# Kernel tuning notes

Measured on AMD Instinct MI355X. Metric: run time of the kernel, lower is better.

The kernel has to match this reference:

```python
import jax, jax.numpy as jnp
import numpy as np

B, E = 256, 512
C, K = 8192, 10          # n_class, n_center
LMD = 10.0
INV_GAMMA = 10.0         # 1 / gamma, gamma = 0.1
TAU = 0.2
MARGIN = 0.01


def setup_inputs() -> dict:
    key = jax.random.key(0)
    k1, k2, k3 = jax.random.split(key, 3)
    embeddings = jax.random.normal(k1, (B, E), dtype=jnp.float32)
    labels = jax.random.randint(k2, (B,), 0, C, dtype=jnp.int64)
    fc = jax.random.normal(k3, (C * K, E), dtype=jnp.float32)
    return {"embeddings": embeddings, "labels": labels, "fc": fc}


def reference(embeddings, labels, fc):
    # L2-normalize centers (rows of fc), like F.normalize(fc, p=2, dim=1)
    norm = jnp.sqrt(jnp.sum(fc * fc, axis=1, keepdims=True))
    w = fc / jnp.maximum(norm, 1e-12)

    # similarity to every center: [B, C, K]
    x = (embeddings @ w.T).reshape(B, C, K)
    prob = jax.nn.softmax(INV_GAMMA * x, axis=2)
    h = jnp.sum(prob * x, axis=2)  # [B, C] soft-pooled class similarity

    # subtract margin on ground-truth class, then cross-entropy
    rows = jnp.arange(B)
    margin_m = jnp.zeros_like(h).at[rows, labels].set(MARGIN)
    logits = LMD * (h - margin_m)
    logp = jax.nn.log_softmax(logits, axis=1)
    loss_cls = -jnp.mean(logp[rows, labels])

    # regularizer: batched per-class center gram, replaces python loop over C
    wc = w.reshape(C, K, E)
    sub = 1.0 - jnp.einsum('cke,cje->ckj', wc, wc)   # [C, K, K]
    sub = jnp.where(sub <= 0.0, 1e-10, sub)
    mask = jnp.triu(jnp.ones((K, K), dtype=bool), k=1)  # strict upper triangle
    safe = jnp.where(mask, 2.0 * sub, 1.0)
    reg = jnp.sum(jnp.where(mask, jnp.sqrt(safe), 0.0))
    reg = reg / (C * K * (K - 1.0))
    return loss_cls + TAU * reg
```

## Files before the change

kernel.cpp:

```cpp
#include <hip/hip_runtime.h>


typedef __bf16 bf16;
typedef bf16 bf16x8 __attribute__((ext_vector_type(8)));
typedef float f32x4 __attribute__((ext_vector_type(4)));

#define NCLASS 8192
#define KC 10
#define EDIM 512
#define BATCH 256

__device__ inline void load_lds16(const void* g, void* l) {
    __builtin_amdgcn_global_load_lds(
        (const __attribute__((address_space(1))) void*)g,
        (__attribute__((address_space(3))) void*)l, 16, 0, 0);
}

__global__ __launch_bounds__(256) void prep_kernel(
    const float* __restrict__ fc, bf16* __restrict__ w,
    float* __restrict__ gram_part)
{
    __shared__ float rows[KC * EDIM];
    __shared__ float s_invn[KC];
    __shared__ float s_wsum[4];
    const int c = blockIdx.x;
    const int t = threadIdx.x;
    const int wave = t >> 6, lane = t & 63;

    const float4* src = (const float4*)(fc + (size_t)c * (KC * EDIM));
    float4* rows4 = (float4*)rows;
    #pragma unroll
    for (int i = 0; i < 5; ++i) rows4[t + i * 256] = src[t + i * 256];
    __syncthreads();

    for (int r = wave; r < KC; r += 4) {
        float s = 0.f;
        #pragma unroll
        for (int j = 0; j < 8; ++j) {
            float v = rows[r * EDIM + lane + j * 64];
            s += v * v;
        }
        #pragma unroll
        for (int off = 32; off; off >>= 1) s += __shfl_xor(s, off);
        if (lane == 0) s_invn[r] = 1.0f / fmaxf(sqrtf(s), 1e-12f);
    }
    __syncthreads();

    bf16x8* dst = (bf16x8*)(w + (size_t)c * (KC * EDIM));
    #pragma unroll
    for (int p = 0; p < 3; ++p) {
        int j = t + p * 256;
        if (j < 640) {
            int r = j >> 6;
            float inv = s_invn[r];
            float4 a = *(const float4*)(rows + j * 8);
            float4 b = *(const float4*)(rows + j * 8 + 4);
            bf16x8 v;
            v[0] = (bf16)(a.x * inv); v[1] = (bf16)(a.y * inv);
            v[2] = (bf16)(a.z * inv); v[3] = (bf16)(a.w * inv);
            v[4] = (bf16)(b.x * inv); v[5] = (bf16)(b.y * inv);
            v[6] = (bf16)(b.z * inv); v[7] = (bf16)(b.w * inv);
            dst[j] = v;
        }
    }

    float part = 0.f;
    for (int p = wave; p < 45; p += 4) {
        int i = 0, pp = p;
        while (pp >= 9 - i) { pp -= 9 - i; ++i; }
        int j = i + 1 + pp;
        float s = 0.f;
        #pragma unroll
        for (int u = 0; u < 8; ++u)
            s += rows[i * EDIM + lane + u * 64] * rows[j * EDIM + lane + u * 64];
        #pragma unroll
        for (int off = 32; off; off >>= 1) s += __shfl_xor(s, off);
        if (lane == 0) {
            float sub = 1.0f - s * s_invn[i] * s_invn[j];
            if (sub <= 0.0f) sub = 1e-10f;
            part += sqrtf(2.0f * sub);
        }
    }
    if (lane == 0) s_wsum[wave] = part;
    __syncthreads();
    if (t == 0) gram_part[c] = s_wsum[0] + s_wsum[1] + s_wsum[2] + s_wsum[3];
}

__global__ __launch_bounds__(256) void conv_kernel(
    const float* __restrict__ e, bf16* __restrict__ At)
{
    int i = blockIdx.x * 256 + threadIdx.x;
    int row = i >> 6, chunk = i & 63;
    int k = chunk * 8;
    float4 a = ((const float4*)e)[i * 2];
    float4 b = ((const float4*)e)[i * 2 + 1];
    bf16x8 v;
    v[0] = (bf16)a.x; v[1] = (bf16)a.y; v[2] = (bf16)a.z; v[3] = (bf16)a.w;
    v[4] = (bf16)b.x; v[5] = (bf16)b.y; v[6] = (bf16)b.z; v[7] = (bf16)b.w;
    *(bf16x8*)&At[((k >> 5) << 13) + (row << 5) + (k & 31)] = v;
}

__global__ __launch_bounds__(512, 2) void gemm_h_kernel(
    const bf16* __restrict__ W,
    const bf16* __restrict__ At,
    float* __restrict__ h)
{
    __shared__ bf16 Ws[80 * 32];
    const int tid = threadIdx.x;
    const int wave = tid >> 6, lane = tid & 63;

    f32x4 acc[5][2];
    #pragma unroll
    for (int mt = 0; mt < 5; ++mt)
        #pragma unroll
        for (int nt = 0; nt < 2; ++nt)
            acc[mt][nt] = (f32x4){0.f, 0.f, 0.f, 0.f};

    const size_t g0 = (size_t)blockIdx.x * 80;

    const int srow = tid >> 2;
    const int gc = (tid & 3) ^ ((srow >> 1) & 3);
    const bf16* wsrc = W + (g0 + srow) * EDIM + gc * 8;

    const int q = lane >> 4;
    const int q8 = q * 8;
    const int fr = lane & 15;

    for (int kb = 0; kb < EDIM; kb += 32) {
        if (tid < 320)
            load_lds16(wsrc + kb, Ws + wave * 64 * 8);
        __syncthreads();

        bf16x8 wf[5], ef[2];
        #pragma unroll
        for (int nt = 0; nt < 2; ++nt) {
            int row = wave * 32 + nt * 16 + fr;
            ef[nt] = *(const bf16x8*)
                &At[((kb >> 5) << 13) + (row << 5) + q8];
        }
        #pragma unroll
        for (int mt = 0; mt < 5; ++mt) {
            int row = mt * 16 + fr;
            int slot = q ^ ((row >> 1) & 3);
            wf[mt] = *(const bf16x8*)&Ws[row * 32 + slot * 8];
        }
        #pragma unroll
        for (int mt = 0; mt < 5; ++mt)
            #pragma unroll
            for (int nt = 0; nt < 2; ++nt)
                acc[mt][nt] = __builtin_amdgcn_mfma_f32_16x16x32_bf16(
                    wf[mt], ef[nt], acc[mt][nt], 0, 0, 0);
        __syncthreads();
    }

    const int col = lane & 15;
    const int quad = lane >> 4;
    const int cb = blockIdx.x * 8;
    #pragma unroll
    for (int nt = 0; nt < 2; ++nt) {
        int b = wave * 32 + nt * 16 + col;
        float hval[8];
        #pragma unroll
        for (int cc = 0; cc < 8; ++cc) {
            float xm = -1e30f;
            #pragma unroll
            for (int mt = 0; mt < 5; ++mt) {
                if (10 * cc + 10 > 16 * mt && 10 * cc < 16 * mt + 16) {
                    #pragma unroll
                    for (int rg = 0; rg < 4; ++rg) {
                        int r = 16 * mt + 4 * quad + rg;
                        if (r >= 10 * cc && r < 10 * cc + 10)
                            xm = fmaxf(xm, acc[mt][nt][rg]);
                    }
                }
            }
            xm = fmaxf(xm, __shfl_xor(xm, 16));
            xm = fmaxf(xm, __shfl_xor(xm, 32));
            float s1 = 0.f, s2 = 0.f;
            #pragma unroll
            for (int mt = 0; mt < 5; ++mt) {
                if (10 * cc + 10 > 16 * mt && 10 * cc < 16 * mt + 16) {
                    #pragma unroll
                    for (int rg = 0; rg < 4; ++rg) {
                        int r = 16 * mt + 4 * quad + rg;
                        if (r >= 10 * cc && r < 10 * cc + 10) {
                            float x = acc[mt][nt][rg];
                            float e = __expf(10.0f * (x - xm));
                            s1 += e; s2 += e * x;
                        }
                    }
                }
            }
            s1 += __shfl_xor(s1, 16); s1 += __shfl_xor(s1, 32);
            s2 += __shfl_xor(s2, 16); s2 += __shfl_xor(s2, 32);
            hval[cc] = s2 / s1;
        }
        if (quad == 0) {
            float4 v0 = {hval[0], hval[1], hval[2], hval[3]};
            float4 v1 = {hval[4], hval[5], hval[6], hval[7]};
            float4* dst = (float4*)&h[(size_t)b * NCLASS + cb];
            dst[0] = v0;
            dst[1] = v1;
        }
    }
}

__global__ __launch_bounds__(256) void ce_kernel(
    const float* __restrict__ h, const int* __restrict__ labels,
    float* __restrict__ ce_part)
{
    __shared__ float redm[4];
    __shared__ float reds[4];
    const int b = blockIdx.x, t = threadIdx.x;
    const int wave = t >> 6, lane = t & 63;
    const int lbl = labels[b];
    const float* hb = h + (size_t)b * NCLASS;

    float lg_cache[32];
    float mx = -1e30f;
    #pragma unroll
    for (int k = 0; k < 32; ++k) {
        int c = t + k * 256;
        float lg = 10.0f * hb[c];
        if (c == lbl) lg -= 0.1f;
        lg_cache[k] = lg;
        mx = fmaxf(mx, lg);
    }
    #pragma unroll
    for (int off = 32; off; off >>= 1) mx = fmaxf(mx, __shfl_xor(mx, off));
    if (lane == 0) redm[wave] = mx;
    __syncthreads();
    mx = fmaxf(fmaxf(redm[0], redm[1]), fmaxf(redm[2], redm[3]));

    float s = 0.f;
    #pragma unroll
    for (int k = 0; k < 32; ++k) s += __expf(lg_cache[k] - mx);
    #pragma unroll
    for (int off = 32; off; off >>= 1) s += __shfl_xor(s, off);
    if (lane == 0) reds[wave] = s;
    __syncthreads();
    if (t == 0) {
        s = reds[0] + reds[1] + reds[2] + reds[3];
        float logit_l = 10.0f * (hb[lbl] - 0.01f);
        ce_part[b] = mx + logf(s) - logit_l;
    }
}

__global__ __launch_bounds__(256) void final_kernel(
    const float* __restrict__ gram_part, const float* __restrict__ ce_part,
    float* __restrict__ out)
{
    __shared__ float red[4];
    const int t = threadIdx.x, wave = t >> 6, lane = t & 63;
    float g = 0.f;
    #pragma unroll
    for (int i = 0; i < 32; ++i) g += gram_part[t + i * 256];
    float val = ce_part[t] * (1.0f / 256.0f)
              + g * (0.2f / 737280.0f);
    #pragma unroll
    for (int off = 32; off; off >>= 1) val += __shfl_xor(val, off);
    if (lane == 0) red[wave] = val;
    __syncthreads();
    if (t == 0) out[0] = red[0] + red[1] + red[2] + red[3];
}

extern "C" void kernel_launch(void* const* d_in, const int* in_sizes, int n_in,
                              void* d_out, int out_size, void* d_ws, size_t ws_size,
                              hipStream_t stream) {
    const float* emb    = (const float*)d_in[0];
    const int*   labels = (const int*)d_in[1];
    const float* fc     = (const float*)d_in[2];
    float* out = (float*)d_out;

    char* ws = (char*)d_ws;
    bf16*  w         = (bf16*)ws;
    bf16*  At        = (bf16*)(ws + 83886080);
    float* h         = (float*)(ws + 84148352);
    float* gram_part = (float*)(ws + 92536960);
    float* ce_part   = (float*)(ws + 92569728);

    prep_kernel<<<NCLASS, 256, 0, stream>>>(fc, w, gram_part);
    conv_kernel<<<64, 256, 0, stream>>>(emb, At);
    gemm_h_kernel<<<81920 / 80, 512, 0, stream>>>(w, At, h);
    ce_kernel<<<BATCH, 256, 0, stream>>>(h, labels, ce_part);
    final_kernel<<<1, 256, 0, stream>>>(gram_part, ce_part, out);
}
```

Before: 302.3 us.

## Double-buffer GEMM LDS tiles, fuse conv into prep, vectorize CE and final loads

The GEMM now stages 64-wide K tiles of W into two LDS buffers with an XOR swizzle, issuing the next tile's async global-to-LDS load before computing on the current one. This halves the barrier count and overlaps loads with MFMA work. The embedding bf16 conversion is folded into the prep kernel as extra blocks, which removes one launch. The CE and final reduction kernels switch to float4 loads. The cost is more LDS per block and more complex swizzle indexing.

```diff
diff --git a/kernel.cpp b/kernel.cpp
--- a/kernel.cpp
+++ b/kernel.cpp
@@ -9,6 +9,7 @@
 #define KC 10
 #define EDIM 512
 #define BATCH 256
+#define BK 64
 
 __device__ inline void load_lds16(const void* g, void* l) {
     __builtin_amdgcn_global_load_lds(
@@ -18,13 +19,28 @@
 
 __global__ __launch_bounds__(256) void prep_kernel(
     const float* __restrict__ fc, bf16* __restrict__ w,
-    float* __restrict__ gram_part)
+    float* __restrict__ gram_part,
+    const float* __restrict__ e, bf16* __restrict__ At)
 {
     __shared__ float rows[KC * EDIM];
     __shared__ float s_invn[KC];
     __shared__ float s_wsum[4];
+    const int t = threadIdx.x;
+
+    if (blockIdx.x >= NCLASS) {
+        int i = (blockIdx.x - NCLASS) * 256 + t;
+        int row = i >> 6, chunk = i & 63;
+        int k = chunk * 8;
+        float4 a = ((const float4*)e)[i * 2];
+        float4 b = ((const float4*)e)[i * 2 + 1];
+        bf16x8 v;
+        v[0] = (bf16)a.x; v[1] = (bf16)a.y; v[2] = (bf16)a.z; v[3] = (bf16)a.w;
+        v[4] = (bf16)b.x; v[5] = (bf16)b.y; v[6] = (bf16)b.z; v[7] = (bf16)b.w;
+        *(bf16x8*)&At[((k >> 5) << 13) + (row << 5) + (k & 31)] = v;
+        return;
+    }
+
     const int c = blockIdx.x;
-    const int t = threadIdx.x;
     const int wave = t >> 6, lane = t & 63;
 
     const float4* src = (const float4*)(fc + (size_t)c * (KC * EDIM));
@@ -86,26 +102,12 @@
     if (t == 0) gram_part[c] = s_wsum[0] + s_wsum[1] + s_wsum[2] + s_wsum[3];
 }
 
-__global__ __launch_bounds__(256) void conv_kernel(
-    const float* __restrict__ e, bf16* __restrict__ At)
-{
-    int i = blockIdx.x * 256 + threadIdx.x;
-    int row = i >> 6, chunk = i & 63;
-    int k = chunk * 8;
-    float4 a = ((const float4*)e)[i * 2];
-    float4 b = ((const float4*)e)[i * 2 + 1];
-    bf16x8 v;
-    v[0] = (bf16)a.x; v[1] = (bf16)a.y; v[2] = (bf16)a.z; v[3] = (bf16)a.w;
-    v[4] = (bf16)b.x; v[5] = (bf16)b.y; v[6] = (bf16)b.z; v[7] = (bf16)b.w;
-    *(bf16x8*)&At[((k >> 5) << 13) + (row << 5) + (k & 31)] = v;
-}
-
 __global__ __launch_bounds__(512, 2) void gemm_h_kernel(
     const bf16* __restrict__ W,
     const bf16* __restrict__ At,
     float* __restrict__ h)
 {
-    __shared__ bf16 Ws[80 * 32];
+    __shared__ bf16 Ws[2][80 * BK];
     const int tid = threadIdx.x;
     const int wave = tid >> 6, lane = tid & 63;
 
@@ -118,38 +120,49 @@
 
     const size_t g0 = (size_t)blockIdx.x * 80;
 
-    const int srow = tid >> 2;
-    const int gc = (tid & 3) ^ ((srow >> 1) & 3);
-    const bf16* wsrc = W + (g0 + srow) * EDIM + gc * 8;
+    const int rA = tid >> 3, sA = tid & 7;
+    const bf16* srcA = W + (g0 + rA) * EDIM + ((sA ^ (rA & 7)) << 3);
+    const int rB = (512 + tid) >> 3, sB = tid & 7;
+    const bf16* srcB = W + (g0 + rB) * EDIM + ((sB ^ (rB & 7)) << 3);
 
     const int q = lane >> 4;
     const int q8 = q * 8;
     const int fr = lane & 15;
 
-    for (int kb = 0; kb < EDIM; kb += 32) {
-        if (tid < 320)
-            load_lds16(wsrc + kb, Ws + wave * 64 * 8);
-        __syncthreads();
-
-        bf16x8 wf[5], ef[2];
-        #pragma unroll
-        for (int nt = 0; nt < 2; ++nt) {
-            int row = wave * 32 + nt * 16 + fr;
-            ef[nt] = *(const bf16x8*)
-                &At[((kb >> 5) << 13) + (row << 5) + q8];
-        }
-        #pragma unroll
-        for (int mt = 0; mt < 5; ++mt) {
-            int row = mt * 16 + fr;
-            int slot = q ^ ((row >> 1) & 3);
-            wf[mt] = *(const bf16x8*)&Ws[row * 32 + slot * 8];
-        }
-        #pragma unroll
-        for (int mt = 0; mt < 5; ++mt)
-            #pragma unroll
-            for (int nt = 0; nt < 2; ++nt)
-                acc[mt][nt] = __builtin_amdgcn_mfma_f32_16x16x32_bf16(
-                    wf[mt], ef[nt], acc[mt][nt], 0, 0, 0);
+    load_lds16(srcA, &Ws[0][wave * 512]);
+    if (tid < 128) load_lds16(srcB, &Ws[0][4096 + wave * 512]);
+    __syncthreads();
+
+    for (int t = 0; t < 8; ++t) {
+        const int cur = t & 1;
+        if (t < 7) {
+            const int kb = (t + 1) * BK;
+            load_lds16(srcA + kb, &Ws[cur ^ 1][wave * 512]);
+            if (tid < 128) load_lds16(srcB + kb, &Ws[cur ^ 1][4096 + wave * 512]);
+        }
+        #pragma unroll
+        for (int kk = 0; kk < BK; kk += 32) {
+            const int ccb = kk >> 3;
+            bf16x8 wf[5], ef[2];
+            #pragma unroll
+            for (int nt = 0; nt < 2; ++nt) {
+                int row = wave * 32 + nt * 16 + fr;
+                ef[nt] = *(const bf16x8*)
+                    &At[((t * 2 + (kk >> 5)) << 13) + (row << 5) + q8];
+            }
+            #pragma unroll
+            for (int mt = 0; mt < 5; ++mt) {
+                int row = mt * 16 + fr;
+                int s = (ccb + q) ^ (row & 7);
+                wf[mt] = *(const bf16x8*)&Ws[cur][row * BK + (s << 3)];
+            }
+            #pragma unroll
+            for (int mt = 0; mt < 5; ++mt)
+                #pragma unroll
+                for (int nt = 0; nt < 2; ++nt)
+                    acc[mt][nt] = __builtin_amdgcn_mfma_f32_16x16x32_bf16(
+                        wf[mt], ef[nt], acc[mt][nt], 0, 0, 0);
+        }
         __syncthreads();
     }
 
@@ -215,16 +228,21 @@
     const int wave = t >> 6, lane = t & 63;
     const int lbl = labels[b];
     const float* hb = h + (size_t)b * NCLASS;
-
-    float lg_cache[32];
+    const float4* hb4 = (const float4*)hb;
+    const int lq = lbl >> 2, lr = lbl & 3;
+
+    float4 v[8];
     float mx = -1e30f;
     #pragma unroll
-    for (int k = 0; k < 32; ++k) {
-        int c = t + k * 256;
-        float lg = 10.0f * hb[c];
-        if (c == lbl) lg -= 0.1f;
-        lg_cache[k] = lg;
-        mx = fmaxf(mx, lg);
+    for (int k = 0; k < 8; ++k) {
+        int idx = t + k * 256;
+        float4 x = hb4[idx];
+        x.x = 10.0f * x.x - ((idx == lq && lr == 0) ? 0.1f : 0.0f);
+        x.y = 10.0f * x.y - ((idx == lq && lr == 1) ? 0.1f : 0.0f);
+        x.z = 10.0f * x.z - ((idx == lq && lr == 2) ? 0.1f : 0.0f);
+        x.w = 10.0f * x.w - ((idx == lq && lr == 3) ? 0.1f : 0.0f);
+        v[k] = x;
+        mx = fmaxf(mx, fmaxf(fmaxf(x.x, x.y), fmaxf(x.z, x.w)));
     }
     #pragma unroll
     for (int off = 32; off; off >>= 1) mx = fmaxf(mx, __shfl_xor(mx, off));
@@ -234,7 +252,10 @@
 
     float s = 0.f;
     #pragma unroll
-    for (int k = 0; k < 32; ++k) s += __expf(lg_cache[k] - mx);
+    for (int k = 0; k < 8; ++k) {
+        s += __expf(v[k].x - mx) + __expf(v[k].y - mx)
+           + __expf(v[k].z - mx) + __expf(v[k].w - mx);
+    }
     #pragma unroll
     for (int off = 32; off; off >>= 1) s += __shfl_xor(s, off);
     if (lane == 0) reds[wave] = s;
@@ -252,9 +273,13 @@
 {
     __shared__ float red[4];
     const int t = threadIdx.x, wave = t >> 6, lane = t & 63;
+    const float4* gp4 = (const float4*)gram_part;
     float g = 0.f;
     #pragma unroll
-    for (int i = 0; i < 32; ++i) g += gram_part[t + i * 256];
+    for (int i = 0; i < 8; ++i) {
+        float4 x = gp4[t + i * 256];
+        g += x.x + x.y + x.z + x.w;
+    }
     float val = ce_part[t] * (1.0f / 256.0f)
               + g * (0.2f / 737280.0f);
     #pragma unroll
@@ -279,8 +304,7 @@
     float* gram_part = (float*)(ws + 92536960);
     float* ce_part   = (float*)(ws + 92569728);
 
-    prep_kernel<<<NCLASS, 256, 0, stream>>>(fc, w, gram_part);
-    conv_kernel<<<64, 256, 0, stream>>>(emb, At);
+    prep_kernel<<<NCLASS + 64, 256, 0, stream>>>(fc, w, gram_part, emb, At);
     gemm_h_kernel<<<81920 / 80, 512, 0, stream>>>(w, At, h);
     ce_kernel<<<BATCH, 256, 0, stream>>>(h, labels, ce_part);
     final_kernel<<<1, 256, 0, stream>>>(gram_part, ce_part, out);
```

Result: no change. 300.2 us (-0.7%).
